# Performance work log

Hardware: AMD Instinct MI355X
Metric: run time of the kernel (lower is better)

## Reference

```python
import jax, jax.numpy as jnp
import numpy as np

B, L, FT, FS, H = 32, 4096, 512, 512, 512  # batch, seq, text feat, summary feat, hidden
C = FT + FS + 1  # conv1 in-channels (num_features + 1 coverage channel)


def setup_inputs() -> dict:
    key = jax.random.key(0)
    ks = jax.random.split(key, 8)
    text_states = jax.random.normal(ks[0], (B, L, FT), dtype=jnp.float32)
    summary_current_state = jax.random.normal(ks[1], (B, FS), dtype=jnp.float32)
    coverage = jax.random.uniform(ks[2], (B, 1, L), dtype=jnp.float32)
    W1 = jax.random.normal(ks[3], (H, C), dtype=jnp.float32) * (1.0 / np.sqrt(C))
    b1 = jnp.zeros((H,), dtype=jnp.float32)
    W2 = jax.random.normal(ks[4], (1, H), dtype=jnp.float32) * (1.0 / np.sqrt(H))
    b2 = jnp.zeros((1,), dtype=jnp.float32)
    text_length = jax.random.randint(ks[5], (B,), 1, L + 1)  # >=1 so softmax is defined
    return {
        "text_states": text_states,
        "summary_current_state": summary_current_state,
        "coverage": coverage,
        "W1": W1,
        "b1": b1,
        "W2": W2,
        "b2": b2,
        "text_length": text_length,
    }


def reference(text_states, summary_current_state, coverage, W1, b1, W2, b2, text_length):
    b, l, ft = text_states.shape
    ts = jnp.swapaxes(text_states, -1, -2)  # [B, FT, L]
    ss = jnp.broadcast_to(summary_current_state[..., None],
                          summary_current_state.shape + (l,))  # [B, FS, L]
    x = jnp.concatenate([ts, ss, coverage], axis=-2)  # [B, C, L]
    # kernel-size-1 Conv1d == pointwise linear over channels
    h = jnp.tanh(jnp.einsum('bcl,hc->bhl', x, W1) + b1[None, :, None])  # [B, H, L]
    logits = jnp.einsum('bhl,oh->bol', h, W2) + b2[None, :, None]  # [B, 1, L]
    mask = jnp.arange(l)[None, None, :] < text_length[:, None, None]  # [B, 1, L]
    masked = jnp.where(mask, logits, -jnp.inf)
    attention = jax.nn.softmax(masked, axis=-1)  # [B, 1, L]
    context_vector = jnp.sum(attention * ts, axis=-1)  # [B, FT]
    return context_vector, attention
```

## Files before the change

kernel.cpp:

```cpp
#include <hip/hip_runtime.h>
#include <cstdint>
#include <cstddef>

#define B_  32
#define L_  4096
#define FT_ 512
#define FS_ 512
#define H_  512
#define C_  1025
#define TL  64
#define NCH (L_ / TL)

typedef __attribute__((ext_vector_type(8))) short short8;
typedef __attribute__((ext_vector_type(4))) float float4v;

__device__ __forceinline__ short f2bf(float f) {
    union { float f; unsigned u; } v; v.f = f;
    unsigned r = v.u + 0x7FFF + ((v.u >> 16) & 1);
    return (short)(r >> 16);
}

__device__ __forceinline__ float fast_tanh(float x) {
    float e = __expf(2.f * x);
    return 1.f - 2.f * __builtin_amdgcn_rcpf(e + 1.f);
}

__global__ __launch_bounds__(256) void prep_kernel(
        const float* __restrict__ W1, const float* __restrict__ summary,
        const float* __restrict__ b1, short* __restrict__ fragB,
        float* __restrict__ w1c, float* __restrict__ sconst) {
    if (blockIdx.x < 128) {
        int gid = blockIdx.x * 256 + threadIdx.x;
        int lane = gid & 63;
        int ts_  = gid >> 6;
        int t = ts_ >> 4;
        int s = ts_ & 15;
        int h  = t * 16 + (lane & 15);
        int k0 = s * 32 + (lane >> 4) * 8;
        const float* src = W1 + (size_t)h * C_ + k0;
        short8 o;
        #pragma unroll
        for (int j = 0; j < 8; ++j) o[j] = f2bf(src[j]);
        *(short8*)(fragB + (size_t)gid * 8) = o;
        if (gid < H_) w1c[gid] = W1[(size_t)gid * C_ + FT_ + FS_];
    } else {
        int wid  = ((blockIdx.x - 128) * 256 + threadIdx.x) >> 6;
        int lane = threadIdx.x & 63;
        int b = wid >> 9;
        int h = wid & 511;
        const float* wrow = W1 + (size_t)h * C_ + FT_;
        const float* srow = summary + (size_t)b * FS_;
        float acc = 0.f;
        #pragma unroll
        for (int f = lane; f < FS_; f += 64) acc += wrow[f] * srow[f];
        #pragma unroll
        for (int off = 32; off > 0; off >>= 1) acc += __shfl_down(acc, off, 64);
        if (lane == 0) sconst[wid] = acc + b1[h];
    }
}

__global__ __launch_bounds__(256, 2) void logits_ctx_kernel(
        const float* __restrict__ ts, const float* __restrict__ coverage,
        const int* __restrict__ text_length,
        const short* __restrict__ fragB, const float* __restrict__ w1c,
        const float* __restrict__ sconst, const float* __restrict__ W2,
        const float* __restrict__ b2, float* __restrict__ logits,
        float2* __restrict__ stats_c, float* __restrict__ cpart) {
    const int b  = blockIdx.y;
    const int l0 = blockIdx.x * TL;
    const int len = text_length[b];
    if (l0 >= len) return;

    __shared__ short ts_lds[TL * 512];

    const float4* src = (const float4*)(ts + ((size_t)b * L_ + l0) * FT_);
    for (int j = threadIdx.x; j < TL * 64; j += 256) {
        int l = j >> 6;
        int g = j & 63;
        float4 v0 = src[2 * j];
        float4 v1 = src[2 * j + 1];
        short8 p;
        p[0] = f2bf(v0.x); p[1] = f2bf(v0.y); p[2] = f2bf(v0.z); p[3] = f2bf(v0.w);
        p[4] = f2bf(v1.x); p[5] = f2bf(v1.y); p[6] = f2bf(v1.z); p[7] = f2bf(v1.w);
        *(short8*)(ts_lds + l * 512 + ((g ^ (l & 7)) << 3)) = p;
    }
    __syncthreads();

    const int lane = threadIdx.x & 63;
    const int wv   = threadIdx.x >> 6;
    const int col  = lane & 15;
    const int quad = lane >> 4;
    const int swz  = col & 7;

    const short* aBase = ts_lds + col * 512;
    const short* bBase = fragB + (size_t)(wv * 8) * 16 * 512 + lane * 8;

    float4v acc[8][4];
    #pragma unroll
    for (int nt = 0; nt < 8; ++nt)
        #pragma unroll
        for (int mt = 0; mt < 4; ++mt)
            acc[nt][mt] = (float4v){0.f, 0.f, 0.f, 0.f};

    for (int ks = 0; ks < 16; ++ks) {
        short8 af[4];
        const int ag = ((ks * 4 + quad) ^ swz) << 3;
        #pragma unroll
        for (int mt = 0; mt < 4; ++mt)
            af[mt] = *(const short8*)(aBase + mt * (16 * 512) + ag);
        #pragma unroll
        for (int nt = 0; nt < 8; ++nt) {
            short8 bf = *(const short8*)(bBase + (size_t)(nt * 16 + ks) * 512);
            #pragma unroll
            for (int mt = 0; mt < 4; ++mt)
                acc[nt][mt] = __builtin_amdgcn_mfma_f32_16x16x32_bf16(
                    af[mt], bf, acc[nt][mt], 0, 0, 0);
        }
    }

    const int h0 = wv * 128;
    const float* sc_b = sconst + (size_t)b * H_;
    float4 cov[4];
    #pragma unroll
    for (int mt = 0; mt < 4; ++mt)
        cov[mt] = *(const float4*)(coverage + (size_t)b * L_ + l0 + mt * 16 + quad * 4);

    float partial[4][4];
    #pragma unroll
    for (int mt = 0; mt < 4; ++mt)
        #pragma unroll
        for (int r = 0; r < 4; ++r) partial[mt][r] = 0.f;

    #pragma unroll
    for (int nt = 0; nt < 8; ++nt) {
        const int h = h0 + nt * 16 + col;
        const float sc = sc_b[h];
        const float wc = w1c[h];
        const float w2 = W2[h];
        #pragma unroll
        for (int mt = 0; mt < 4; ++mt)
            #pragma unroll
            for (int r = 0; r < 4; ++r) {
                float pre = acc[nt][mt][r] + sc + wc * ((const float*)&cov[mt])[r];
                partial[mt][r] += w2 * fast_tanh(pre);
            }
    }

    #pragma unroll
    for (int mt = 0; mt < 4; ++mt)
        #pragma unroll
        for (int r = 0; r < 4; ++r) {
            float v = partial[mt][r];
            v += __shfl_xor(v, 8, 64);
            v += __shfl_xor(v, 4, 64);
            v += __shfl_xor(v, 2, 64);
            v += __shfl_xor(v, 1, 64);
            partial[mt][r] = v;
        }

    __syncthreads();
    float* red  = (float*)ts_lds;
    float* wbuf = red + 256;
    if (col == 0) {
        #pragma unroll
        for (int mt = 0; mt < 4; ++mt)
            #pragma unroll
            for (int r = 0; r < 4; ++r)
                red[wv * 64 + mt * 16 + quad * 4 + r] = partial[mt][r];
    }
    __syncthreads();

    if (threadIdx.x < 64) {
        const int t = threadIdx.x;
        const bool valid = (l0 + t < len);
        float lg = b2[0];
        #pragma unroll
        for (int w = 0; w < 4; ++w) lg += red[w * 64 + t];
        logits[(size_t)b * L_ + l0 + t] = lg;
        float mv = valid ? lg : -INFINITY;
        #pragma unroll
        for (int off = 32; off > 0; off >>= 1)
            mv = fmaxf(mv, __shfl_xor(mv, off, 64));
        const float wt = valid ? __expf(lg - mv) : 0.f;
        float sv = wt;
        #pragma unroll
        for (int off = 32; off > 0; off >>= 1) sv += __shfl_xor(sv, off, 64);
        wbuf[t] = wt;
        if (t == 0) {
            float2 o; o.x = mv; o.y = sv;
            stats_c[(size_t)b * NCH + blockIdx.x] = o;
        }
    }
    __syncthreads();

    const int lend = min(len - l0, TL);
    const float* tsbase = ts + ((size_t)b * L_ + l0) * FT_ + 2 * threadIdx.x;
    float cx = 0.f, cy = 0.f;
    for (int l = 0; l < lend; ++l) {
        const float wl = wbuf[l];
        const float2 v = *(const float2*)(tsbase + (size_t)l * FT_);
        cx += wl * v.x; cy += wl * v.y;
    }
    float2 o; o.x = cx; o.y = cy;
    *(float2*)(cpart + ((size_t)b * NCH + blockIdx.x) * FT_ + 2 * threadIdx.x) = o;
}

__global__ __launch_bounds__(512) void finalize_kernel(
        const float* __restrict__ logits, const float2* __restrict__ stats_c,
        const float* __restrict__ cpart, const int* __restrict__ text_length,
        float* __restrict__ ctx, float* __restrict__ attn_out) {
    const int b   = blockIdx.x;
    const int len = text_length[b];
    const int nv  = (len + TL - 1) / TL;
    const int t   = threadIdx.x;
    __shared__ float sm[NCH];
    __shared__ float redm[8];
    __shared__ float reds[8];

    float2 st; st.x = 0.f; st.y = 0.f;
    float mloc = -INFINITY;
    if (t < nv) { st = stats_c[(size_t)b * NCH + t]; mloc = st.x; }
    float v = mloc;
    #pragma unroll
    for (int off = 32; off > 0; off >>= 1) v = fmaxf(v, __shfl_xor(v, off, 64));
    if ((t & 63) == 0) redm[t >> 6] = v;
    __syncthreads();
    float m = redm[0];
    #pragma unroll
    for (int w = 1; w < 8; ++w) m = fmaxf(m, redm[w]);

    float sume = 0.f;
    if (t < nv) {
        const float sc = __expf(st.x - m);
        sm[t] = sc;
        sume = st.y * sc;
    }
    float sv = sume;
    #pragma unroll
    for (int off = 32; off > 0; off >>= 1) sv += __shfl_xor(sv, off, 64);
    if ((t & 63) == 0) reds[t >> 6] = sv;
    __syncthreads();
    float tot = 0.f;
    #pragma unroll
    for (int w = 0; w < 8; ++w) tot += reds[w];
    const float inv = 1.f / tot;

    const float* lgrow = logits + (size_t)b * L_;
    float* arow = attn_out + (size_t)b * L_;
    #pragma unroll
    for (int i = 0; i < L_ / 512; ++i) {
        const int l = i * 512 + t;
        float a = 0.f;
        if (l < len) a = __expf(lgrow[l] - m) * inv;
        arow[l] = a;
    }

    const float* cp = cpart + (size_t)b * NCH * FT_ + t;
    float c = 0.f;
    #pragma unroll 4
    for (int ch = 0; ch < nv; ++ch) c += sm[ch] * cp[(size_t)ch * FT_];
    ctx[(size_t)b * FT_ + t] = c * inv;
}

extern "C" void kernel_launch(void* const* d_in, const int* in_sizes, int n_in,
                              void* d_out, int out_size, void* d_ws, size_t ws_size,
                              hipStream_t stream) {
    const float* ts       = (const float*)d_in[0];
    const float* summary  = (const float*)d_in[1];
    const float* coverage = (const float*)d_in[2];
    const float* W1       = (const float*)d_in[3];
    const float* b1       = (const float*)d_in[4];
    const float* W2       = (const float*)d_in[5];
    const float* b2       = (const float*)d_in[6];
    const int*   text_len = (const int*)d_in[7];

    float* ctx_out  = (float*)d_out;
    float* attn_out = (float*)d_out + B_ * FT_;

    char* ws = (char*)d_ws;
    short*  fragB   = (short*)(ws);
    float*  w1c     = (float*)(ws + 524288);
    float*  sconst  = (float*)(ws + 526336);
    float*  logits  = (float*)(ws + 591872);
    float2* stats_c = (float2*)(ws + 1116160);
    float*  cpart   = (float*)(ws + 1132544);

    prep_kernel<<<128 + 4096, 256, 0, stream>>>(W1, summary, b1, fragB, w1c, sconst);
    logits_ctx_kernel<<<dim3(NCH, B_), 256, 0, stream>>>(
        ts, coverage, text_len, fragB, w1c, sconst, W2, b2, logits, stats_c, cpart);
    finalize_kernel<<<B_, 512, 0, stream>>>(
        logits, stats_c, cpart, text_len, ctx_out, attn_out);
}
```

Baseline: 464.8 us.

## Use 512-thread blocks with 8 waves splitting H and prefetch B fragments

Doubles the block to 8 waves so each wave computes 64 hidden units instead of 128, halving per-wave accumulators, and raises the launch-bounds occupancy target. The B-fragment loads from global memory are software-pipelined one k-step ahead of the MFMAs. The context accumulation now has each thread handle one feature instead of two. The intent is better latency hiding and occupancy, at the cost of LDS A-fragments being re-read by twice as many waves and more block-level synchronisation.

```diff
diff --git a/kernel.cpp b/kernel.cpp
--- a/kernel.cpp
+++ b/kernel.cpp
@@ -59,7 +59,7 @@
     }
 }
 
-__global__ __launch_bounds__(256, 2) void logits_ctx_kernel(
+__global__ __launch_bounds__(512, 4) void logits_ctx_kernel(
         const float* __restrict__ ts, const float* __restrict__ coverage,
         const int* __restrict__ text_length,
         const short* __restrict__ fragB, const float* __restrict__ w1c,
@@ -74,7 +74,7 @@
     __shared__ short ts_lds[TL * 512];
 
     const float4* src = (const float4*)(ts + ((size_t)b * L_ + l0) * FT_);
-    for (int j = threadIdx.x; j < TL * 64; j += 256) {
+    for (int j = threadIdx.x; j < TL * 64; j += 512) {
         int l = j >> 6;
         int g = j & 63;
         float4 v0 = src[2 * j];
@@ -93,32 +93,63 @@
     const int swz  = col & 7;
 
     const short* aBase = ts_lds + col * 512;
-    const short* bBase = fragB + (size_t)(wv * 8) * 16 * 512 + lane * 8;
-
-    float4v acc[8][4];
-    #pragma unroll
-    for (int nt = 0; nt < 8; ++nt)
+    const short* bBase = fragB + (size_t)(wv * 4) * 16 * 512 + lane * 8;
+
+#define LDB(ntv, ksv) (*(const short8*)(bBase + (size_t)((ntv) * 16 + (ksv)) * 512))
+
+    float4v acc[4][4];
+    #pragma unroll
+    for (int nt = 0; nt < 4; ++nt)
         #pragma unroll
         for (int mt = 0; mt < 4; ++mt)
             acc[nt][mt] = (float4v){0.f, 0.f, 0.f, 0.f};
 
-    for (int ks = 0; ks < 16; ++ks) {
+    short8 bc0 = LDB(0, 0), bc1 = LDB(1, 0), bc2 = LDB(2, 0), bc3 = LDB(3, 0);
+
+    for (int ks = 0; ks < 15; ++ks) {
         short8 af[4];
         const int ag = ((ks * 4 + quad) ^ swz) << 3;
         #pragma unroll
         for (int mt = 0; mt < 4; ++mt)
             af[mt] = *(const short8*)(aBase + mt * (16 * 512) + ag);
-        #pragma unroll
-        for (int nt = 0; nt < 8; ++nt) {
-            short8 bf = *(const short8*)(bBase + (size_t)(nt * 16 + ks) * 512);
-            #pragma unroll
-            for (int mt = 0; mt < 4; ++mt)
-                acc[nt][mt] = __builtin_amdgcn_mfma_f32_16x16x32_bf16(
-                    af[mt], bf, acc[nt][mt], 0, 0, 0);
-        }
-    }
-
-    const int h0 = wv * 128;
+        short8 bn0 = LDB(0, ks + 1), bn1 = LDB(1, ks + 1),
+               bn2 = LDB(2, ks + 1), bn3 = LDB(3, ks + 1);
+        #pragma unroll
+        for (int mt = 0; mt < 4; ++mt)
+            acc[0][mt] = __builtin_amdgcn_mfma_f32_16x16x32_bf16(af[mt], bc0, acc[0][mt], 0, 0, 0);
+        #pragma unroll
+        for (int mt = 0; mt < 4; ++mt)
+            acc[1][mt] = __builtin_amdgcn_mfma_f32_16x16x32_bf16(af[mt], bc1, acc[1][mt], 0, 0, 0);
+        #pragma unroll
+        for (int mt = 0; mt < 4; ++mt)
+            acc[2][mt] = __builtin_amdgcn_mfma_f32_16x16x32_bf16(af[mt], bc2, acc[2][mt], 0, 0, 0);
+        #pragma unroll
+        for (int mt = 0; mt < 4; ++mt)
+            acc[3][mt] = __builtin_amdgcn_mfma_f32_16x16x32_bf16(af[mt], bc3, acc[3][mt], 0, 0, 0);
+        bc0 = bn0; bc1 = bn1; bc2 = bn2; bc3 = bn3;
+    }
+    {
+        short8 af[4];
+        const int ag = ((15 * 4 + quad) ^ swz) << 3;
+        #pragma unroll
+        for (int mt = 0; mt < 4; ++mt)
+            af[mt] = *(const short8*)(aBase + mt * (16 * 512) + ag);
+        #pragma unroll
+        for (int mt = 0; mt < 4; ++mt)
+            acc[0][mt] = __builtin_amdgcn_mfma_f32_16x16x32_bf16(af[mt], bc0, acc[0][mt], 0, 0, 0);
+        #pragma unroll
+        for (int mt = 0; mt < 4; ++mt)
+            acc[1][mt] = __builtin_amdgcn_mfma_f32_16x16x32_bf16(af[mt], bc1, acc[1][mt], 0, 0, 0);
+        #pragma unroll
+        for (int mt = 0; mt < 4; ++mt)
+            acc[2][mt] = __builtin_amdgcn_mfma_f32_16x16x32_bf16(af[mt], bc2, acc[2][mt], 0, 0, 0);
+        #pragma unroll
+        for (int mt = 0; mt < 4; ++mt)
+            acc[3][mt] = __builtin_amdgcn_mfma_f32_16x16x32_bf16(af[mt], bc3, acc[3][mt], 0, 0, 0);
+    }
+#undef LDB
+
+    const int h0 = wv * 64;
     const float* sc_b = sconst + (size_t)b * H_;
     float4 cov[4];
     #pragma unroll
@@ -132,7 +163,7 @@
         for (int r = 0; r < 4; ++r) partial[mt][r] = 0.f;
 
     #pragma unroll
-    for (int nt = 0; nt < 8; ++nt) {
+    for (int nt = 0; nt < 4; ++nt) {
         const int h = h0 + nt * 16 + col;
         const float sc = sc_b[h];
         const float wc = w1c[h];
@@ -160,7 +191,7 @@
 
     __syncthreads();
     float* red  = (float*)ts_lds;
-    float* wbuf = red + 256;
+    float* wbuf = red + 512;
     if (col == 0) {
         #pragma unroll
         for (int mt = 0; mt < 4; ++mt)
@@ -175,7 +206,7 @@
         const bool valid = (l0 + t < len);
         float lg = b2[0];
         #pragma unroll
-        for (int w = 0; w < 4; ++w) lg += red[w * 64 + t];
+        for (int w = 0; w < 8; ++w) lg += red[w * 64 + t];
         logits[(size_t)b * L_ + l0 + t] = lg;
         float mv = valid ? lg : -INFINITY;
         #pragma unroll
@@ -194,15 +225,11 @@
     __syncthreads();
 
     const int lend = min(len - l0, TL);
-    const float* tsbase = ts + ((size_t)b * L_ + l0) * FT_ + 2 * threadIdx.x;
-    float cx = 0.f, cy = 0.f;
-    for (int l = 0; l < lend; ++l) {
-        const float wl = wbuf[l];
-        const float2 v = *(const float2*)(tsbase + (size_t)l * FT_);
-        cx += wl * v.x; cy += wl * v.y;
-    }
-    float2 o; o.x = cx; o.y = cy;
-    *(float2*)(cpart + ((size_t)b * NCH + blockIdx.x) * FT_ + 2 * threadIdx.x) = o;
+    const float* tsb = ts + ((size_t)b * L_ + l0) * FT_ + threadIdx.x;
+    float cx = 0.f;
+    #pragma unroll 4
+    for (int l = 0; l < lend; ++l) cx += wbuf[l] * tsb[(size_t)l * FT_];
+    cpart[((size_t)b * NCH + blockIdx.x) * FT_ + threadIdx.x] = cx;
 }
 
 __global__ __launch_bounds__(512) void finalize_kernel(
@@ -286,7 +313,7 @@
     float*  cpart   = (float*)(ws + 1132544);
 
     prep_kernel<<<128 + 4096, 256, 0, stream>>>(W1, summary, b1, fragB, w1c, sconst);
-    logits_ctx_kernel<<<dim3(NCH, B_), 256, 0, stream>>>(
+    logits_ctx_kernel<<<dim3(NCH, B_), 512, 0, stream>>>(
         ts, coverage, text_len, fragB, w1c, sconst, W2, b2, logits, stats_c, cpart);
     finalize_kernel<<<B_, 512, 0, stream>>>(
         logits, stats_c, cpart, text_len, ctx_out, attn_out);
```

Result: faster. 429.4 us (-7.6%).
